# Kernel tuning notes

Hardware: AMD Instinct MI355X
Metric: run time of the kernel (lower is better)

## Reference

```python
import jax, jax.numpy as jnp
import numpy as np

B, T, DM, DFE, DH, DRH = 32, 2048, 128, 64, 64, 64
E, NF, NSF, TOPK = 8, 16, 64, 2
LN_EPS = 1e-5


def setup_inputs() -> dict:
    key = jax.random.key(0)
    ks = jax.random.split(key, 18)
    s = 0.05
    # base expert i owns columns [16*i, 16*i+16); scale=2 -> expert e uses base e//2
    expert_idx = jnp.asarray(np.stack([np.arange(NF) + NF * (e // 2) for e in range(E)]), dtype=jnp.int32)  # [E,NF]
    stage_idx = jnp.arange(NSF, dtype=jnp.int32)  # stage uses all 64 columns
    return {
        'hidden': jax.random.normal(ks[0], (B, T, DM), jnp.float32),
        'feat': jax.random.normal(ks[1], (B, T, NSF), jnp.float32),
        'ln_g': jnp.ones((DM,), jnp.float32),
        'ln_b': jnp.zeros((DM,), jnp.float32),
        'Wp': jax.random.normal(ks[2], (NSF, DFE), jnp.float32) * s,
        'bp': jnp.zeros((DFE,), jnp.float32),
        'Wr1': jax.random.normal(ks[3], (DM + DFE, DRH), jnp.float32) * s,
        'br1': jnp.zeros((DRH,), jnp.float32),
        'Wr2': jax.random.normal(ks[4], (DRH, E), jnp.float32) * s,
        'br2': jnp.zeros((E,), jnp.float32),
        'Wf': jax.random.normal(ks[5], (E, NF, DFE), jnp.float32) * s,
        'bf': jnp.zeros((E, DFE), jnp.float32),
        'We1h': jax.random.normal(ks[6], (E, DM, DH), jnp.float32) * s,
        'We1f': jax.random.normal(ks[7], (E, DFE, DH), jnp.float32) * s,
        'be1': jnp.zeros((E, DH), jnp.float32),
        'We2': jax.random.normal(ks[8], (E, DH, DM), jnp.float32) * s,
        'be2': jnp.zeros((E, DM), jnp.float32),
        'alpha': jnp.asarray(1.0, jnp.float32),
        'item_seq_len': jax.random.randint(ks[9], (B,), 1, T + 1),
        'expert_idx': expert_idx,
        'stage_idx': stage_idx,
    }


def _layernorm(x, g, b):
    mu = jnp.mean(x, -1, keepdims=True)
    v = jnp.mean(jnp.square(x - mu), -1, keepdims=True)
    return (x - mu) * jax.lax.rsqrt(v + LN_EPS) * g + b


def reference(hidden, feat, ln_g, ln_b, Wp, bp, Wr1, br1, Wr2, br2,
              Wf, bf, We1h, We1f, be1, We2, be2, alpha,
              item_seq_len, expert_idx, stage_idx):
    h = _layernorm(hidden, ln_g, ln_b)                         # [B,T,DM]  pre_ln
    femb = feat[..., stage_idx] @ Wp + bp                      # [B,T,DFE] stage feature projection
    # --- token router: MLP -> softmax(temp=1) -> top-k renormalized gates ---
    rin = jnp.concatenate([h, femb], -1)                       # [B,T,DM+DFE]
    logits = jax.nn.relu(rin @ Wr1 + br1) @ Wr2 + br2          # [B,T,E]
    probs = jax.nn.softmax(logits, axis=-1)
    topv, topi = jax.lax.top_k(probs, TOPK)                    # [B,T,K]
    topv = topv / jnp.sum(topv, -1, keepdims=True)
    gates = jnp.sum(jax.nn.one_hot(topi, E, dtype=probs.dtype) * topv[..., None], axis=-2)  # [B,T,E]
    valid = jnp.arange(T)[None, :] < item_seq_len[:, None]     # [B,T]
    gates = gates * valid[..., None].astype(gates.dtype)
    # --- experts: per-expert feature gather + 2-layer GELU MLP (hidden + feat inputs) ---
    ef = feat[:, :, expert_idx]                                # [B,T,E,NF] gather
    x = jnp.einsum('btef,efd->bted', ef, Wf) + bf              # [B,T,E,DFE]
    h1 = jax.nn.gelu(jnp.einsum('btd,edo->bteo', h, We1h)
                     + jnp.einsum('bted,edo->bteo', x, We1f) + be1, approximate=False)
    eo = jnp.einsum('bteo,eod->bted', h1, We2) + be2           # [B,T,E,DM]
    moe = jnp.einsum('bte,bted->btd', gates, eo)               # weighted combine
    next_hidden = hidden + alpha * moe                         # residual, alpha_scale=1, dropout=0
    return next_hidden, gates, probs
```

## Files before the change

kernel.cpp:

```cpp
#include <hip/hip_runtime.h>
#include <hip/hip_bf16.h>


typedef unsigned short u16;
typedef __attribute__((ext_vector_type(8))) short bfrag;
typedef __attribute__((ext_vector_type(8))) u16 u16x8;
typedef __attribute__((ext_vector_type(4))) float facc;
typedef __attribute__((ext_vector_type(4))) float f32x4;

#define NTOK 65536
#define CAP 65536

#define OFF_CNT   ((size_t)0)
#define OFF_FLG   ((size_t)64)
#define OFF_LTOK  ((size_t)512)
#define OFF_SMAPG (OFF_LTOK + (size_t)8*CAP*4)
#define OFF_HWS   (OFF_SMAPG + (size_t)NTOK*8)
#define OFF_EOTOK (OFF_HWS + (size_t)NTOK*128*2)
#define OFF_W1T   (OFF_EOTOK + (size_t)NTOK*2*128*2)
#define OFF_W2T   (OFF_W1T + 163840)
#define OFF_B1P   (OFF_W2T + 131072)
#define OFF_WPR   (OFF_B1P + 2048)
#define OFF_BR1P  (OFF_WPR + 16384)

__device__ __forceinline__ u16 f2bf(float f) {
  union { __hip_bfloat16 h; u16 u; } cv;
  cv.h = __float2bfloat16(f);
  return cv.u;
}
__device__ __forceinline__ float bf2f(u16 u) {
  return __uint_as_float(((unsigned)u) << 16);
}

__global__ __launch_bounds__(256)
void k0a_pre(const float* __restrict__ Wp, const float* __restrict__ bp,
             const float* __restrict__ Wr1, const float* __restrict__ br1,
             const float* __restrict__ Wf, const float* __restrict__ bfv,
             const float* __restrict__ We1h, const float* __restrict__ We1f,
             const float* __restrict__ be1, const float* __restrict__ We2,
             const int* __restrict__ eidx_g, const int* __restrict__ sidx_g,
             float* __restrict__ Wpr, float* __restrict__ br1p,
             u16* __restrict__ w1t, u16* __restrict__ w2t, float* __restrict__ b1p,
             int* __restrict__ flags)
{
  __shared__ float smA[64*68];
  __shared__ float smB[128*68];
  int b = blockIdx.x, tid = threadIdx.x;

  if (b == 0) {
    for (int idx = tid; idx < 4096; idx += 256) {
      int r = idx >> 6, c = idx & 63;
      smA[r*68 + c] = Wp[idx];
      smB[r*68 + c] = Wr1[128*64 + idx];
    }
    if (tid == 0) { int ok = 1; for (int i = 0; i < 64; ++i) ok &= (sidx_g[i] == i); flags[0] = ok; }
    __syncthreads();
    int i = tid >> 2, oq = (tid & 3) * 16;
    f32x4 acc[4];
    #pragma unroll
    for (int m = 0; m < 4; ++m) { f32x4 z = {0,0,0,0}; acc[m] = z; }
    for (int k = 0; k < 64; ++k) {
      float a = smA[i*68 + k];
      #pragma unroll
      for (int m = 0; m < 4; ++m) {
        f32x4 b4 = *(const f32x4*)(smB + k*68 + oq + m*4);
        #pragma unroll
        for (int j = 0; j < 4; ++j) acc[m][j] = fmaf(a, b4[j], acc[m][j]);
      }
    }
    #pragma unroll
    for (int m = 0; m < 4; ++m) *(f32x4*)(Wpr + i*64 + oq + m*4) = acc[m];
    if (tid < 64) {
      float s = br1[tid];
      for (int k = 0; k < 64; ++k) s = fmaf(bp[k], smB[k*68 + tid], s);
      br1p[tid] = s;
    }
  } else if (b <= 8) {
    int e = b - 1;
    for (int idx = tid; idx < 4096; idx += 256) {
      int r = idx >> 6, c = idx & 63;
      smB[r*68 + c] = We1f[e*4096 + idx];
    }
    for (int idx = tid; idx < 1024; idx += 256) {
      int r = idx >> 6, c = idx & 63;
      smA[r*68 + c] = Wf[e*1024 + idx];
    }
    if (tid == 0) {
      int s0 = eidx_g[e*16]; int ok = 1;
      for (int i = 0; i < 16; ++i) ok &= (eidx_g[e*16 + i] == s0 + i);
      flags[1 + e] = ok ? s0 : -1;
    }
    __syncthreads();
    int i = tid >> 4, jq = (tid & 15) * 4;
    f32x4 acc = {0,0,0,0};
    for (int d = 0; d < 64; ++d) {
      float a = smA[i*68 + d];
      f32x4 b4 = *(const f32x4*)(smB + d*68 + jq);
      #pragma unroll
      for (int j = 0; j < 4; ++j) acc[j] = fmaf(a, b4[j], acc[j]);
    }
    #pragma unroll
    for (int j = 0; j < 4; ++j) w1t[(size_t)(e*64 + jq + j)*160 + 128 + i] = f2bf(acc[j]);
    if (tid < 64) {
      float s = be1[e*64 + tid];
      for (int d = 0; d < 64; ++d) s = fmaf(bfv[e*64 + d], smB[d*68 + tid], s);
      b1p[e*64 + tid] = s;
    }
    for (int idx = tid; idx < 1024; idx += 256) {
      int jj = idx >> 4, kk = idx & 15;
      w1t[(size_t)(e*64 + jj)*160 + 144 + kk] = 0;
    }
  } else if (b <= 16) {
    int e = b - 9;
    for (int idx = tid; idx < 8192; idx += 256) {
      int r = idx >> 6, c = idx & 63;
      smB[r*68 + c] = We1h[(size_t)e*8192 + idx];
    }
    __syncthreads();
    int jj = tid & 63, kb = (tid >> 6) * 32;
    #pragma unroll
    for (int m = 0; m < 4; ++m) {
      u16x8 o;
      #pragma unroll
      for (int q = 0; q < 8; ++q) o[q] = f2bf(smB[(kb + m*8 + q)*68 + jj]);
      *(u16x8*)(w1t + (size_t)(e*64 + jj)*160 + kb + m*8) = o;
    }
  } else if (b <= 24) {
    int e = b - 17;
    for (int idx = tid; idx < 8192; idx += 256) {
      int r = idx >> 7, c = idx & 127;
      smB[r*132 + c] = We2[(size_t)e*8192 + idx];
    }
    __syncthreads();
    int d = tid & 127, kb = (tid >> 7) * 32;
    #pragma unroll
    for (int m = 0; m < 4; ++m) {
      u16x8 o;
      #pragma unroll
      for (int q = 0; q < 8; ++q) o[q] = f2bf(smB[(kb + m*8 + q)*132 + d]);
      *(u16x8*)(w2t + (size_t)(e*128 + d)*64 + kb + m*8) = o;
    }
  }
}

__global__ __launch_bounds__(256, 3)
void k1_router(const float* __restrict__ hidden, const float* __restrict__ feat,
               const float* __restrict__ ln_g, const float* __restrict__ ln_b,
               const float* __restrict__ Wr1, const float* __restrict__ Wr2,
               const float* __restrict__ br2, const int* __restrict__ seqlen,
               const int* __restrict__ sidx_g,
               const float* __restrict__ Wpr, const float* __restrict__ br1p,
               const int* __restrict__ flags,
               float* __restrict__ outG, float* __restrict__ outP,
               u16* __restrict__ hws, int* __restrict__ cnt,
               int* __restrict__ listTok, float* __restrict__ smapG)
{
  __shared__ __align__(16) char smemAt[64*128*4];
  __shared__ float Wc[64*64];
  __shared__ float sg[128], sb[128], sb1[64], sbr2[8];
  __shared__ int ssidx[64];
  __shared__ int lcnt[8], lbase[8];
  float* At = (float*)smemAt;
  int* ltok = (int*)smemAt;
  float* tgp = (float*)(smemAt + 4096);

  int tid = threadIdx.x;

  f32x4 wpf[4];
  #pragma unroll
  for (int u = 0; u < 4; ++u) wpf[u] = ((const f32x4*)Wpr)[u*256 + tid];

  if (tid < 128) sg[tid] = ln_g[tid]; else sb[tid-128] = ln_b[tid-128];
  if (tid < 64) { sb1[tid] = br1p[tid]; ssidx[tid] = sidx_g[tid]; }
  if (tid >= 64 && tid < 72) sbr2[tid-64] = br2[tid-64];
  if (tid >= 72 && tid < 80) lcnt[tid-72] = 0;
  int sidok = flags[0];

  int tl = tid >> 1, hq = tid & 1;
  int t = blockIdx.x * 128 + tl;

  f32x4 x[16];
  #pragma unroll
  for (int i = 0; i < 16; ++i) x[i] = *(const f32x4*)(hidden + (size_t)t*128 + hq*64 + i*4);
  float s = 0.f;
  #pragma unroll
  for (int i = 0; i < 16; ++i) { s += x[i][0] + x[i][1]; s += x[i][2] + x[i][3]; }
  s += __shfl_xor(s, 1, 64);
  float mu = s * (1.f/128.f);
  float v = 0.f;
  #pragma unroll
  for (int i = 0; i < 16; ++i) {
    #pragma unroll
    for (int j = 0; j < 4; ++j) { float d = x[i][j] - mu; v = fmaf(d, d, v); }
  }
  v += __shfl_xor(v, 1, 64);
  float rs = rsqrtf(v * (1.f/128.f) + 1e-5f);
  #pragma unroll
  for (int i = 0; i < 16; ++i) {
    #pragma unroll
    for (int j = 0; j < 4; ++j) {
      int c = hq*64 + i*4 + j;
      x[i][j] = (x[i][j] - mu) * rs * sg[c] + sb[c];
    }
  }
  #pragma unroll
  for (int m = 0; m < 8; ++m) {
    u16x8 o;
    #pragma unroll
    for (int j = 0; j < 4; ++j) { o[j] = f2bf(x[2*m][j]); o[4+j] = f2bf(x[2*m+1][j]); }
    *(u16x8*)(hws + (size_t)t*128 + hq*64 + m*8) = o;
  }
  int tb8 = tl >> 3, t7 = (tl & 7) << 2;
  if (sidok) {
    #pragma unroll
    for (int m = 0; m < 8; ++m) {
      f32x4 fv = *(const f32x4*)(feat + (size_t)t*64 + hq*32 + m*4);
      #pragma unroll
      for (int j = 0; j < 4; ++j) {
        int kr = hq*32 + m*4 + j;
        *(float*)((char*)At + (kr << 9) + (((tb8 ^ (kr & 15)) & 15) << 5) + t7) = fv[j];
      }
    }
  } else {
    #pragma unroll
    for (int i = 0; i < 32; ++i) {
      int kr = hq*32 + i;
      float fv = feat[(size_t)t*64 + ssidx[kr]];
      *(float*)((char*)At + (kr << 9) + (((tb8 ^ (kr & 15)) & 15) << 5) + t7) = fv;
    }
  }

  float acc[8][4];
  #pragma unroll
  for (int i = 0; i < 8; ++i)
    #pragma unroll
    for (int p = 0; p < 4; ++p) acc[i][p] = 0.f;

  int g8 = tid >> 4;
  int ob = (tid & 15) * 4;

  #pragma unroll 1
  for (int ci = 0; ci < 3; ++ci) {
    if (ci == 1 && hq == 0) {
      #pragma unroll
      for (int i = 0; i < 16; ++i)
        #pragma unroll
        for (int j = 0; j < 4; ++j) {
          int kr = i*4 + j;
          *(float*)((char*)At + (kr << 9) + (((tb8 ^ (kr & 15)) & 15) << 5) + t7) = x[i][j];
        }
    }
    if (ci == 2 && hq == 1) {
      #pragma unroll
      for (int i = 0; i < 16; ++i)
        #pragma unroll
        for (int j = 0; j < 4; ++j) {
          int kr = i*4 + j;
          *(float*)((char*)At + (kr << 9) + (((tb8 ^ (kr & 15)) & 15) << 5) + t7) = x[i][j];
        }
    }
    #pragma unroll
    for (int u = 0; u < 4; ++u) ((f32x4*)Wc)[u*256 + tid] = wpf[u];
    __syncthreads();
    if (ci < 2) {
      const f32x4* nsrc = (ci == 0) ? (const f32x4*)Wr1 : (const f32x4*)(Wr1 + 4096);
      #pragma unroll
      for (int u = 0; u < 4; ++u) wpf[u] = nsrc[u*256 + tid];
    }
    #pragma unroll 4
    for (int k = 0; k < 64; ++k) {
      int base = (k << 7) + (((g8 ^ (k & 15)) & 15) << 3);
      f32x4 a0 = *(const f32x4*)(At + base);
      f32x4 a1 = *(const f32x4*)(At + base + 4);
      f32x4 b4 = *(const f32x4*)(Wc + k*64 + ob);
      #pragma unroll
      for (int i = 0; i < 4; ++i)
        #pragma unroll
        for (int p = 0; p < 4; ++p) {
          acc[i][p]   = fmaf(a0[i], b4[p], acc[i][p]);
          acc[4+i][p] = fmaf(a1[i], b4[p], acc[4+i][p]);
        }
    }
    __syncthreads();
  }

  float w2r[4][8];
  #pragma unroll
  for (int p = 0; p < 4; ++p) {
    f32x4 wlo = *(const f32x4*)(Wr2 + (ob + p)*8);
    f32x4 whi = *(const f32x4*)(Wr2 + (ob + p)*8 + 4);
    #pragma unroll
    for (int e = 0; e < 4; ++e) { w2r[p][e] = wlo[e]; w2r[p][4+e] = whi[e]; }
  }
  float b1r[4];
  #pragma unroll
  for (int p = 0; p < 4; ++p) b1r[p] = sb1[ob + p];

  int j16 = tid & 15;
  #pragma unroll 1
  for (int ti = 0; ti < 8; ++ti) {
    float lo[8];
    #pragma unroll
    for (int e = 0; e < 8; ++e) lo[e] = 0.f;
    #pragma unroll
    for (int p = 0; p < 4; ++p) {
      float z = fmaxf(acc[ti][p] + b1r[p], 0.f);
      #pragma unroll
      for (int e = 0; e < 8; ++e) lo[e] = fmaf(z, w2r[p][e], lo[e]);
    }
    #pragma unroll
    for (int m = 1; m < 16; m <<= 1) {
      #pragma unroll
      for (int e = 0; e < 8; ++e) lo[e] += __shfl_xor(lo[e], m, 64);
    }
    #pragma unroll
    for (int e = 0; e < 8; ++e) lo[e] += sbr2[e];

    int tloc = g8*8 + ti;
    int tt = blockIdx.x*128 + tloc;
    float mx = lo[0];
    #pragma unroll
    for (int e = 1; e < 8; ++e) mx = fmaxf(mx, lo[e]);
    float ex[8]; float ss = 0.f;
    #pragma unroll
    for (int e = 0; e < 8; ++e) { ex[e] = __expf(lo[e] - mx); ss += ex[e]; }
    float inv = 1.f / ss;
    float p[8];
    #pragma unroll
    for (int e = 0; e < 8; ++e) p[e] = ex[e] * inv;
    float p1 = p[0]; int i1 = 0;
    #pragma unroll
    for (int e = 1; e < 8; ++e) { bool tk2 = p[e] > p1; p1 = tk2 ? p[e] : p1; i1 = tk2 ? e : i1; }
    float p2 = -1.f; int i2 = 0;
    #pragma unroll
    for (int e = 0; e < 8; ++e) { bool tk2 = (e != i1) && (p[e] > p2); p2 = tk2 ? p[e] : p2; i2 = tk2 ? e : i2; }
    bool valid = (tt & 2047) < seqlen[tt >> 11];
    float gden = 1.f / (p1 + p2);
    float g1 = p1 * gden, g2 = p2 * gden;
    float pv = p[0];
    #pragma unroll
    for (int e = 1; e < 8; ++e) pv = (j16 == e) ? p[e] : pv;
    if (j16 < 8) outP[(size_t)tt*8 + j16] = pv;
    float gv = (j16 == i1) ? g1 : ((j16 == i2) ? g2 : 0.f);
    if (!valid) gv = 0.f;
    if (j16 < 8) outG[(size_t)tt*8 + j16] = gv;
    if (j16 == 0) {
      if (valid) {
        int lp = atomicAdd(&lcnt[i1], 1); if (lp < 128) ltok[i1*128 + lp] = (tt << 1);
        lp = atomicAdd(&lcnt[i2], 1);     if (lp < 128) ltok[i2*128 + lp] = (tt << 1) | 1;
        tgp[tloc*2] = g1; tgp[tloc*2+1] = g2;
      } else {
        tgp[tloc*2] = 0.f; tgp[tloc*2+1] = 0.f;
      }
    }
  }

  __syncthreads();
  if (tid < 8) { int n8 = min(lcnt[tid], 128); lbase[tid] = atomicAdd(&cnt[tid], n8); }
  __syncthreads();
  #pragma unroll 1
  for (int e = 0; e < 8; ++e) {
    int ncnt = min(lcnt[e], 128);
    if (tid < ncnt) listTok[(size_t)e*CAP + lbase[e] + tid] = ltok[e*128 + tid];
  }
  if (tid < 128) {
    float2 g; g.x = tgp[tid*2]; g.y = tgp[tid*2+1];
    ((float2*)smapG)[blockIdx.x*128 + tid] = g;
  }
}

__global__ __launch_bounds__(256)
void k2_experts(const float* __restrict__ feat, const u16* __restrict__ hws,
                const u16* __restrict__ w1t, const u16* __restrict__ w2t,
                const float* __restrict__ b1p, const float* __restrict__ be2,
                const int* __restrict__ eidx_g, const int* __restrict__ cnt,
                const int* __restrict__ listTok, const int* __restrict__ flags,
                u16* __restrict__ eoTok)
{
  __shared__ u16 Xs[64*168];
  __shared__ u16 H1s[64*88];
  __shared__ float b1s[64], be2s[128];
  __shared__ int sent[64];
  __shared__ int seidx[16];
  __shared__ int snr;

  int b = blockIdx.x, tid = threadIdx.x;
  int e = -1, row0 = 0, n = 0, accb = 0;
  #pragma unroll
  for (int i = 0; i < 8; ++i) {
    int ci = cnt[i]; int ns = (ci + 63) >> 6;
    if (e < 0 && b < accb + ns) { e = i; row0 = (b - accb) << 6; n = ci; }
    accb += ns;
  }
  if (e < 0) return;
  int nr = n - row0; if (nr > 64) nr = 64;
  if (tid == 0) snr = nr;
  int fb = flags[1 + e];

  if (tid < 64) {
    int ent = (tid < nr) ? listTok[(size_t)e*CAP + row0 + tid] : 0;
    sent[tid] = ent;
    b1s[tid] = b1p[e*64 + tid];
  } else if (tid < 192) {
    be2s[tid - 64] = be2[e*128 + tid - 64];
  } else if (tid < 208) {
    seidx[tid-192] = eidx_g[e*16 + tid - 192];
  }
  __syncthreads();

  for (int c2 = tid; c2 < 1024; c2 += 256) {
    int r = c2 >> 4, p = c2 & 15;
    u16x8 vv = *(const u16x8*)(hws + (size_t)(sent[r] >> 1)*128 + p*8);
    *(u16x8*)((char*)Xs + r*336 + p*16) = vv;
  }
  if (tid < 128) {
    int r = tid >> 1, hf = tid & 1;
    int tk = sent[r] >> 1;
    u16x8 ov;
    if (fb >= 0) {
      f32x4 v0 = *(const f32x4*)(feat + (size_t)tk*64 + fb + hf*8);
      f32x4 v1 = *(const f32x4*)(feat + (size_t)tk*64 + fb + hf*8 + 4);
      #pragma unroll
      for (int q = 0; q < 4; ++q) { ov[q] = f2bf(v0[q]); ov[4+q] = f2bf(v1[q]); }
    } else {
      #pragma unroll
      for (int q = 0; q < 8; ++q) ov[q] = f2bf(feat[(size_t)tk*64 + seidx[hf*8 + q]]);
    }
    *(u16x8*)((char*)Xs + r*336 + 256 + hf*16) = ov;
    u16x8 zv = {0,0,0,0,0,0,0,0};
    *(u16x8*)((char*)Xs + r*336 + 288 + hf*16) = zv;
  }
  __syncthreads();

  int w = tid >> 6, lane = tid & 63;
  int la = lane & 15, lg = lane >> 4;
  const u16* w1e = w1t + (size_t)e*64*160;
  const u16* w2e = w2t + (size_t)e*128*64;

  facc acc[4];
  #pragma unroll
  for (int ni = 0; ni < 4; ++ni) { facc z = {0.f,0.f,0.f,0.f}; acc[ni] = z; }
  #pragma unroll
  for (int kc = 0; kc < 5; ++kc) {
    int r = w*16 + la;
    bfrag af = *(const bfrag*)((const char*)Xs + r*336 + kc*64 + lg*16);
    #pragma unroll
    for (int ni = 0; ni < 4; ++ni) {
      bfrag bf2 = *(const bfrag*)(w1e + (size_t)(ni*16 + la)*160 + kc*32 + lg*8);
      acc[ni] = __builtin_amdgcn_mfma_f32_16x16x32_bf16(af, bf2, acc[ni], 0, 0, 0);
    }
  }
  #pragma unroll
  for (int ni = 0; ni < 4; ++ni)
    #pragma unroll
    for (int rg = 0; rg < 4; ++rg) {
      int r = w*16 + lg*4 + rg;
      int c = ni*16 + la;
      float z = acc[ni][rg] + b1s[c];
      float gl = 0.5f * z * (1.f + erff(z * 0.70710678118f));
      *(u16*)((char*)H1s + r*176 + c*2) = f2bf(gl);
    }
  __syncthreads();

  facc acc2[8];
  #pragma unroll
  for (int ni = 0; ni < 8; ++ni) { facc z = {0.f,0.f,0.f,0.f}; acc2[ni] = z; }
  #pragma unroll
  for (int kc = 0; kc < 2; ++kc) {
    int r = w*16 + la;
    bfrag af = *(const bfrag*)((const char*)H1s + r*176 + kc*64 + lg*16);
    #pragma unroll
    for (int ni = 0; ni < 8; ++ni) {
      bfrag bf2 = *(const bfrag*)(w2e + (size_t)(ni*16 + la)*64 + kc*32 + lg*8);
      acc2[ni] = __builtin_amdgcn_mfma_f32_16x16x32_bf16(af, bf2, acc2[ni], 0, 0, 0);
    }
  }
  #pragma unroll
  for (int ni = 0; ni < 8; ++ni)
    #pragma unroll
    for (int rg = 0; rg < 4; ++rg) {
      int r = w*16 + lg*4 + rg;
      int c = ni*16 + la;
      if (r < snr) {
        float vv = acc2[ni][rg] + be2s[c];
        eoTok[(size_t)sent[r]*128 + c] = f2bf(vv);
      }
    }
}

__global__ __launch_bounds__(256)
void k3_combine(const float* __restrict__ hidden, const float* __restrict__ smapG,
                const u16* __restrict__ eoTok, const float* __restrict__ alphap,
                float* __restrict__ outN)
{
  int tid = threadIdx.x;
  int tok = tid >> 2, q = tid & 3;
  int t = blockIdx.x*64 + tok;
  float2 g = ((const float2*)smapG)[t];
  float a = alphap[0];
  float ag0 = a * g.x, ag1 = a * g.y;
  const f32x4* hp = (const f32x4*)(hidden + (size_t)t*128 + q*32);
  f32x4* op = (f32x4*)(outN + (size_t)t*128 + q*32);
  const u16x8* e0 = (const u16x8*)(eoTok + ((size_t)t*2)*128 + q*32);
  const u16x8* e1 = (const u16x8*)(eoTok + ((size_t)t*2 + 1)*128 + q*32);
  #pragma unroll
  for (int i = 0; i < 4; ++i) {
    f32x4 r0 = hp[2*i], r1 = hp[2*i+1];
    if (g.x != 0.f) {
      u16x8 x0 = e0[i];
      #pragma unroll
      for (int j = 0; j < 4; ++j) { r0[j] = fmaf(ag0, bf2f(x0[j]), r0[j]); r1[j] = fmaf(ag0, bf2f(x0[4+j]), r1[j]); }
    }
    if (g.y != 0.f) {
      u16x8 x1 = e1[i];
      #pragma unroll
      for (int j = 0; j < 4; ++j) { r0[j] = fmaf(ag1, bf2f(x1[j]), r0[j]); r1[j] = fmaf(ag1, bf2f(x1[4+j]), r1[j]); }
    }
    op[2*i] = r0; op[2*i+1] = r1;
  }
}

extern "C" void kernel_launch(void* const* d_in, const int* in_sizes, int n_in,
                              void* d_out, int out_size, void* d_ws, size_t ws_size,
                              hipStream_t stream) {
  const float* hidden = (const float*)d_in[0];
  const float* feat   = (const float*)d_in[1];
  const float* ln_g   = (const float*)d_in[2];
  const float* ln_b   = (const float*)d_in[3];
  const float* Wp     = (const float*)d_in[4];
  const float* bp     = (const float*)d_in[5];
  const float* Wr1    = (const float*)d_in[6];
  const float* br1    = (const float*)d_in[7];
  const float* Wr2    = (const float*)d_in[8];
  const float* br2    = (const float*)d_in[9];
  const float* Wf     = (const float*)d_in[10];
  const float* bfv    = (const float*)d_in[11];
  const float* We1h   = (const float*)d_in[12];
  const float* We1f   = (const float*)d_in[13];
  const float* be1    = (const float*)d_in[14];
  const float* We2    = (const float*)d_in[15];
  const float* be2    = (const float*)d_in[16];
  const float* alpha  = (const float*)d_in[17];
  const int* seqlen   = (const int*)d_in[18];
  const int* eidx     = (const int*)d_in[19];
  const int* sidx     = (const int*)d_in[20];

  char* ws = (char*)d_ws;
  int*   cnt      = (int*)(ws + OFF_CNT);
  int*   flags    = (int*)(ws + OFF_FLG);
  int*   listTok  = (int*)(ws + OFF_LTOK);
  float* smapG    = (float*)(ws + OFF_SMAPG);
  u16*   hws      = (u16*)(ws + OFF_HWS);
  u16*   eoTok    = (u16*)(ws + OFF_EOTOK);
  u16*   w1t      = (u16*)(ws + OFF_W1T);
  u16*   w2t      = (u16*)(ws + OFF_W2T);
  float* b1p      = (float*)(ws + OFF_B1P);
  float* Wpr      = (float*)(ws + OFF_WPR);
  float* br1p     = (float*)(ws + OFF_BR1P);

  float* outN = (float*)d_out;
  float* outG = outN + (size_t)NTOK * 128;
  float* outP = outG + (size_t)NTOK * 8;

  hipMemsetAsync(ws + OFF_CNT, 0, 256, stream);
  k0a_pre<<<25, 256, 0, stream>>>(Wp, bp, Wr1, br1, Wf, bfv, We1h, We1f, be1, We2,
                                  eidx, sidx, Wpr, br1p, w1t, w2t, b1p, flags);
  k1_router<<<512, 256, 0, stream>>>(hidden, feat, ln_g, ln_b, Wr1, Wr2, br2, seqlen,
                                     sidx, Wpr, br1p, flags, outG, outP, hws, cnt,
                                     listTok, smapG);
  k2_experts<<<2056, 256, 0, stream>>>(feat, hws, w1t, w2t, b1p, be2, eidx,
                                       cnt, listTok, flags, eoTok);
  k3_combine<<<1024, 256, 0, stream>>>(hidden, smapG, eoTok, alpha, outN);
}
```

Baseline: 135.0 us.

## Restructure router kernel to 64 tokens per block with split-K across waves

The router kernel now handles 64 tokens per block instead of 128 and launches twice as many blocks. Each wave owns 16 of the 64 hidden units and reads its weights straight from global memory instead of staging them in shared memory. Partial logits from the four waves are reduced through shared memory, and a single wave then does softmax, top-k and vectorized output writes. The aim is higher occupancy and less shared-memory and shuffle traffic. The costs are repeated global or L2 weight loads in every block and an epilogue where only one wave is busy.

```diff
diff --git a/kernel.cpp b/kernel.cpp
--- a/kernel.cpp
+++ b/kernel.cpp
@@ -143,7 +143,7 @@
   }
 }
 
-__global__ __launch_bounds__(256, 3)
+__global__ __launch_bounds__(256, 4)
 void k1_router(const float* __restrict__ hidden, const float* __restrict__ feat,
                const float* __restrict__ ln_g, const float* __restrict__ ln_b,
                const float* __restrict__ Wr1, const float* __restrict__ Wr2,
@@ -155,217 +155,201 @@
                u16* __restrict__ hws, int* __restrict__ cnt,
                int* __restrict__ listTok, float* __restrict__ smapG)
 {
-  __shared__ __align__(16) char smemAt[64*128*4];
-  __shared__ float Wc[64*64];
-  __shared__ float sg[128], sb[128], sb1[64], sbr2[8];
+  __shared__ float At[64*64];
+  __shared__ float plo[64*33 + 4];
+  __shared__ float sg[128], sb[128];
   __shared__ int ssidx[64];
   __shared__ int lcnt[8], lbase[8];
-  float* At = (float*)smemAt;
-  int* ltok = (int*)smemAt;
-  float* tgp = (float*)(smemAt + 4096);
+  __shared__ int ltok[8][64];
 
   int tid = threadIdx.x;
-
-  f32x4 wpf[4];
-  #pragma unroll
-  for (int u = 0; u < 4; ++u) wpf[u] = ((const f32x4*)Wpr)[u*256 + tid];
-
   if (tid < 128) sg[tid] = ln_g[tid]; else sb[tid-128] = ln_b[tid-128];
-  if (tid < 64) { sb1[tid] = br1p[tid]; ssidx[tid] = sidx_g[tid]; }
-  if (tid >= 64 && tid < 72) sbr2[tid-64] = br2[tid-64];
-  if (tid >= 72 && tid < 80) lcnt[tid-72] = 0;
+  if (tid < 64) ssidx[tid] = sidx_g[tid];
+  if (tid >= 128 && tid < 136) lcnt[tid-128] = 0;
   int sidok = flags[0];
 
-  int tl = tid >> 1, hq = tid & 1;
-  int t = blockIdx.x * 128 + tl;
-
-  f32x4 x[16];
-  #pragma unroll
-  for (int i = 0; i < 16; ++i) x[i] = *(const f32x4*)(hidden + (size_t)t*128 + hq*64 + i*4);
+  int tok = tid >> 2, q = tid & 3;
+  int t = blockIdx.x * 64 + tok;
+
+  f32x4 x[8];
+  #pragma unroll
+  for (int i = 0; i < 8; ++i) x[i] = *(const f32x4*)(hidden + (size_t)t*128 + q*32 + i*4);
   float s = 0.f;
   #pragma unroll
-  for (int i = 0; i < 16; ++i) { s += x[i][0] + x[i][1]; s += x[i][2] + x[i][3]; }
-  s += __shfl_xor(s, 1, 64);
+  for (int i = 0; i < 8; ++i) { s += x[i][0] + x[i][1]; s += x[i][2] + x[i][3]; }
+  s += __shfl_xor(s, 1, 64); s += __shfl_xor(s, 2, 64);
   float mu = s * (1.f/128.f);
   float v = 0.f;
   #pragma unroll
-  for (int i = 0; i < 16; ++i) {
+  for (int i = 0; i < 8; ++i) {
     #pragma unroll
     for (int j = 0; j < 4; ++j) { float d = x[i][j] - mu; v = fmaf(d, d, v); }
   }
-  v += __shfl_xor(v, 1, 64);
+  v += __shfl_xor(v, 1, 64); v += __shfl_xor(v, 2, 64);
   float rs = rsqrtf(v * (1.f/128.f) + 1e-5f);
   #pragma unroll
-  for (int i = 0; i < 16; ++i) {
+  for (int i = 0; i < 8; ++i) {
     #pragma unroll
     for (int j = 0; j < 4; ++j) {
-      int c = hq*64 + i*4 + j;
+      int c = q*32 + i*4 + j;
       x[i][j] = (x[i][j] - mu) * rs * sg[c] + sb[c];
     }
   }
   #pragma unroll
-  for (int m = 0; m < 8; ++m) {
+  for (int m = 0; m < 4; ++m) {
     u16x8 o;
     #pragma unroll
     for (int j = 0; j < 4; ++j) { o[j] = f2bf(x[2*m][j]); o[4+j] = f2bf(x[2*m+1][j]); }
-    *(u16x8*)(hws + (size_t)t*128 + hq*64 + m*8) = o;
-  }
-  int tb8 = tl >> 3, t7 = (tl & 7) << 2;
+    *(u16x8*)(hws + (size_t)t*128 + q*32 + m*8) = o;
+  }
+  float fv[16];
   if (sidok) {
     #pragma unroll
-    for (int m = 0; m < 8; ++m) {
-      f32x4 fv = *(const f32x4*)(feat + (size_t)t*64 + hq*32 + m*4);
+    for (int m = 0; m < 4; ++m) {
+      f32x4 f4 = *(const f32x4*)(feat + (size_t)t*64 + q*16 + m*4);
+      #pragma unroll
+      for (int j = 0; j < 4; ++j) fv[m*4+j] = f4[j];
+    }
+  } else {
+    #pragma unroll
+    for (int i = 0; i < 16; ++i) fv[i] = feat[(size_t)t*64 + ssidx[q*16 + i]];
+  }
+
+  int lane = tid & 63;
+  int w = tid >> 6;
+  int wo = __builtin_amdgcn_readfirstlane(w * 16);
+
+  float acc[16];
+  #pragma unroll
+  for (int j = 0; j < 16; ++j) acc[j] = 0.f;
+
+  #pragma unroll 1
+  for (int c = 0; c < 3; ++c) {
+    if (c == 0) {
+      if (q < 2) {
+        #pragma unroll
+        for (int i = 0; i < 8; ++i)
+          #pragma unroll
+          for (int j = 0; j < 4; ++j) {
+            int r = q*32 + i*4 + j;
+            At[(r << 6) + (tok ^ r)] = x[i][j];
+          }
+      }
+    } else if (c == 1) {
+      if (q >= 2) {
+        #pragma unroll
+        for (int i = 0; i < 8; ++i)
+          #pragma unroll
+          for (int j = 0; j < 4; ++j) {
+            int r = (q-2)*32 + i*4 + j;
+            At[(r << 6) + (tok ^ r)] = x[i][j];
+          }
+      }
+    } else {
+      #pragma unroll
+      for (int i = 0; i < 16; ++i) {
+        int r = q*16 + i;
+        At[(r << 6) + (tok ^ r)] = fv[i];
+      }
+    }
+    __syncthreads();
+    const float* wsrc = (c == 0) ? Wr1 : (c == 1) ? (Wr1 + 4096) : Wpr;
+    #pragma unroll 16
+    for (int k = 0; k < 64; ++k) {
+      float xk = At[(k << 6) + (lane ^ k)];
+      const f32x4* wr = (const f32x4*)(wsrc + (k << 6) + wo);
+      f32x4 w0 = wr[0], w1 = wr[1], w2 = wr[2], w3 = wr[3];
       #pragma unroll
       for (int j = 0; j < 4; ++j) {
-        int kr = hq*32 + m*4 + j;
-        *(float*)((char*)At + (kr << 9) + (((tb8 ^ (kr & 15)) & 15) << 5) + t7) = fv[j];
-      }
-    }
-  } else {
-    #pragma unroll
-    for (int i = 0; i < 32; ++i) {
-      int kr = hq*32 + i;
-      float fv = feat[(size_t)t*64 + ssidx[kr]];
-      *(float*)((char*)At + (kr << 9) + (((tb8 ^ (kr & 15)) & 15) << 5) + t7) = fv;
-    }
-  }
-
-  float acc[8][4];
-  #pragma unroll
-  for (int i = 0; i < 8; ++i)
-    #pragma unroll
-    for (int p = 0; p < 4; ++p) acc[i][p] = 0.f;
-
-  int g8 = tid >> 4;
-  int ob = (tid & 15) * 4;
-
-  #pragma unroll 1
-  for (int ci = 0; ci < 3; ++ci) {
-    if (ci == 1 && hq == 0) {
-      #pragma unroll
-      for (int i = 0; i < 16; ++i)
-        #pragma unroll
-        for (int j = 0; j < 4; ++j) {
-          int kr = i*4 + j;
-          *(float*)((char*)At + (kr << 9) + (((tb8 ^ (kr & 15)) & 15) << 5) + t7) = x[i][j];
-        }
-    }
-    if (ci == 2 && hq == 1) {
-      #pragma unroll
-      for (int i = 0; i < 16; ++i)
-        #pragma unroll
-        for (int j = 0; j < 4; ++j) {
-          int kr = i*4 + j;
-          *(float*)((char*)At + (kr << 9) + (((tb8 ^ (kr & 15)) & 15) << 5) + t7) = x[i][j];
-        }
-    }
-    #pragma unroll
-    for (int u = 0; u < 4; ++u) ((f32x4*)Wc)[u*256 + tid] = wpf[u];
+        acc[j]    = fmaf(w0[j], xk, acc[j]);
+        acc[4+j]  = fmaf(w1[j], xk, acc[4+j]);
+        acc[8+j]  = fmaf(w2[j], xk, acc[8+j]);
+        acc[12+j] = fmaf(w3[j], xk, acc[12+j]);
+      }
+    }
     __syncthreads();
-    if (ci < 2) {
-      const f32x4* nsrc = (ci == 0) ? (const f32x4*)Wr1 : (const f32x4*)(Wr1 + 4096);
-      #pragma unroll
-      for (int u = 0; u < 4; ++u) wpf[u] = nsrc[u*256 + tid];
-    }
-    #pragma unroll 4
-    for (int k = 0; k < 64; ++k) {
-      int base = (k << 7) + (((g8 ^ (k & 15)) & 15) << 3);
-      f32x4 a0 = *(const f32x4*)(At + base);
-      f32x4 a1 = *(const f32x4*)(At + base + 4);
-      f32x4 b4 = *(const f32x4*)(Wc + k*64 + ob);
-      #pragma unroll
-      for (int i = 0; i < 4; ++i)
-        #pragma unroll
-        for (int p = 0; p < 4; ++p) {
-          acc[i][p]   = fmaf(a0[i], b4[p], acc[i][p]);
-          acc[4+i][p] = fmaf(a1[i], b4[p], acc[4+i][p]);
-        }
-    }
-    __syncthreads();
-  }
-
-  float w2r[4][8];
-  #pragma unroll
-  for (int p = 0; p < 4; ++p) {
-    f32x4 wlo = *(const f32x4*)(Wr2 + (ob + p)*8);
-    f32x4 whi = *(const f32x4*)(Wr2 + (ob + p)*8 + 4);
-    #pragma unroll
-    for (int e = 0; e < 4; ++e) { w2r[p][e] = wlo[e]; w2r[p][4+e] = whi[e]; }
-  }
-  float b1r[4];
-  #pragma unroll
-  for (int p = 0; p < 4; ++p) b1r[p] = sb1[ob + p];
-
-  int j16 = tid & 15;
-  #pragma unroll 1
-  for (int ti = 0; ti < 8; ++ti) {
+  }
+
+  {
     float lo[8];
     #pragma unroll
     for (int e = 0; e < 8; ++e) lo[e] = 0.f;
-    #pragma unroll
-    for (int p = 0; p < 4; ++p) {
-      float z = fmaxf(acc[ti][p] + b1r[p], 0.f);
-      #pragma unroll
-      for (int e = 0; e < 8; ++e) lo[e] = fmaf(z, w2r[p][e], lo[e]);
-    }
-    #pragma unroll
-    for (int m = 1; m < 16; m <<= 1) {
-      #pragma unroll
-      for (int e = 0; e < 8; ++e) lo[e] += __shfl_xor(lo[e], m, 64);
-    }
-    #pragma unroll
-    for (int e = 0; e < 8; ++e) lo[e] += sbr2[e];
-
-    int tloc = g8*8 + ti;
-    int tt = blockIdx.x*128 + tloc;
-    float mx = lo[0];
-    #pragma unroll
-    for (int e = 1; e < 8; ++e) mx = fmaxf(mx, lo[e]);
+    const f32x4* b1v = (const f32x4*)(br1p + wo);
+    f32x4 b0 = b1v[0], b1 = b1v[1], b2 = b1v[2], b3 = b1v[3];
+    #pragma unroll
+    for (int j = 0; j < 16; ++j) {
+      float bj = (j < 4) ? b0[j & 3] : (j < 8) ? b1[j & 3] : (j < 12) ? b2[j & 3] : b3[j & 3];
+      float zj = fmaxf(acc[j] + bj, 0.f);
+      const f32x4* w2p = (const f32x4*)(Wr2 + (wo + j)*8);
+      f32x4 wa = w2p[0], wb = w2p[1];
+      #pragma unroll
+      for (int e = 0; e < 4; ++e) {
+        lo[e]   = fmaf(zj, wa[e], lo[e]);
+        lo[4+e] = fmaf(zj, wb[e], lo[4+e]);
+      }
+    }
+    #pragma unroll
+    for (int e = 0; e < 8; ++e) plo[lane*33 + w*8 + e] = lo[e];
+  }
+  __syncthreads();
+
+  if (w == 0) {
+    int tt = blockIdx.x*64 + lane;
+    float L[8];
+    #pragma unroll
+    for (int e = 0; e < 8; ++e)
+      L[e] = plo[lane*33 + e] + plo[lane*33 + 8 + e] + plo[lane*33 + 16 + e]
+           + plo[lane*33 + 24 + e] + br2[e];
+    float mx = L[0];
+    #pragma unroll
+    for (int e = 1; e < 8; ++e) mx = fmaxf(mx, L[e]);
     float ex[8]; float ss = 0.f;
     #pragma unroll
-    for (int e = 0; e < 8; ++e) { ex[e] = __expf(lo[e] - mx); ss += ex[e]; }
+    for (int e = 0; e < 8; ++e) { ex[e] = __expf(L[e] - mx); ss += ex[e]; }
     float inv = 1.f / ss;
     float p[8];
     #pragma unroll
     for (int e = 0; e < 8; ++e) p[e] = ex[e] * inv;
     float p1 = p[0]; int i1 = 0;
     #pragma unroll
-    for (int e = 1; e < 8; ++e) { bool tk2 = p[e] > p1; p1 = tk2 ? p[e] : p1; i1 = tk2 ? e : i1; }
+    for (int e = 1; e < 8; ++e) { bool tk = p[e] > p1; p1 = tk ? p[e] : p1; i1 = tk ? e : i1; }
     float p2 = -1.f; int i2 = 0;
     #pragma unroll
-    for (int e = 0; e < 8; ++e) { bool tk2 = (e != i1) && (p[e] > p2); p2 = tk2 ? p[e] : p2; i2 = tk2 ? e : i2; }
+    for (int e = 0; e < 8; ++e) { bool tk = (e != i1) && (p[e] > p2); p2 = tk ? p[e] : p2; i2 = tk ? e : i2; }
     bool valid = (tt & 2047) < seqlen[tt >> 11];
     float gden = 1.f / (p1 + p2);
     float g1 = p1 * gden, g2 = p2 * gden;
-    float pv = p[0];
-    #pragma unroll
-    for (int e = 1; e < 8; ++e) pv = (j16 == e) ? p[e] : pv;
-    if (j16 < 8) outP[(size_t)tt*8 + j16] = pv;
-    float gv = (j16 == i1) ? g1 : ((j16 == i2) ? g2 : 0.f);
-    if (!valid) gv = 0.f;
-    if (j16 < 8) outG[(size_t)tt*8 + j16] = gv;
-    if (j16 == 0) {
-      if (valid) {
-        int lp = atomicAdd(&lcnt[i1], 1); if (lp < 128) ltok[i1*128 + lp] = (tt << 1);
-        lp = atomicAdd(&lcnt[i2], 1);     if (lp < 128) ltok[i2*128 + lp] = (tt << 1) | 1;
-        tgp[tloc*2] = g1; tgp[tloc*2+1] = g2;
-      } else {
-        tgp[tloc*2] = 0.f; tgp[tloc*2+1] = 0.f;
-      }
-    }
-  }
-
+
+    f32x4 pa, pb;
+    #pragma unroll
+    for (int e = 0; e < 4; ++e) { pa[e] = p[e]; pb[e] = p[4+e]; }
+    *(f32x4*)(outP + (size_t)tt*8)     = pa;
+    *(f32x4*)(outP + (size_t)tt*8 + 4) = pb;
+
+    f32x4 ga, gb;
+    #pragma unroll
+    for (int e = 0; e < 4; ++e) {
+      ga[e] = valid ? ((e == i1) ? g1 : (e == i2) ? g2 : 0.f) : 0.f;
+      gb[e] = valid ? ((e+4 == i1) ? g1 : (e+4 == i2) ? g2 : 0.f) : 0.f;
+    }
+    *(f32x4*)(outG + (size_t)tt*8)     = ga;
+    *(f32x4*)(outG + (size_t)tt*8 + 4) = gb;
+
+    float2 gm; gm.x = valid ? g1 : 0.f; gm.y = valid ? g2 : 0.f;
+    ((float2*)smapG)[tt] = gm;
+
+    if (valid) {
+      int lp = atomicAdd(&lcnt[i1], 1); ltok[i1][lp] = (tt << 1);
+      lp = atomicAdd(&lcnt[i2], 1);     ltok[i2][lp] = (tt << 1) | 1;
+    }
+  }
   __syncthreads();
-  if (tid < 8) { int n8 = min(lcnt[tid], 128); lbase[tid] = atomicAdd(&cnt[tid], n8); }
+  if (tid < 8) lbase[tid] = atomicAdd(&cnt[tid], lcnt[tid]);
   __syncthreads();
   #pragma unroll 1
   for (int e = 0; e < 8; ++e) {
-    int ncnt = min(lcnt[e], 128);
-    if (tid < ncnt) listTok[(size_t)e*CAP + lbase[e] + tid] = ltok[e*128 + tid];
-  }
-  if (tid < 128) {
-    float2 g; g.x = tgp[tid*2]; g.y = tgp[tid*2+1];
-    ((float2*)smapG)[blockIdx.x*128 + tid] = g;
+    int ncnt = lcnt[e];
+    if (tid < ncnt) listTok[(size_t)e*CAP + lbase[e] + tid] = ltok[e][tid];
   }
 }
 
@@ -421,10 +405,10 @@
       f32x4 v0 = *(const f32x4*)(feat + (size_t)tk*64 + fb + hf*8);
       f32x4 v1 = *(const f32x4*)(feat + (size_t)tk*64 + fb + hf*8 + 4);
       #pragma unroll
-      for (int q = 0; q < 4; ++q) { ov[q] = f2bf(v0[q]); ov[4+q] = f2bf(v1[q]); }
+      for (int p = 0; p < 4; ++p) { ov[p] = f2bf(v0[p]); ov[4+p] = f2bf(v1[p]); }
     } else {
       #pragma unroll
-      for (int q = 0; q < 8; ++q) ov[q] = f2bf(feat[(size_t)tk*64 + seidx[hf*8 + q]]);
+      for (int p = 0; p < 8; ++p) ov[p] = f2bf(feat[(size_t)tk*64 + seidx[hf*8 + p]]);
     }
     *(u16x8*)((char*)Xs + r*336 + 256 + hf*16) = ov;
     u16x8 zv = {0,0,0,0,0,0,0,0};
@@ -565,9 +549,9 @@
   hipMemsetAsync(ws + OFF_CNT, 0, 256, stream);
   k0a_pre<<<25, 256, 0, stream>>>(Wp, bp, Wr1, br1, Wf, bfv, We1h, We1f, be1, We2,
                                   eidx, sidx, Wpr, br1p, w1t, w2t, b1p, flags);
-  k1_router<<<512, 256, 0, stream>>>(hidden, feat, ln_g, ln_b, Wr1, Wr2, br2, seqlen,
-                                     sidx, Wpr, br1p, flags, outG, outP, hws, cnt,
-                                     listTok, smapG);
+  k1_router<<<1024, 256, 0, stream>>>(hidden, feat, ln_g, ln_b, Wr1, Wr2, br2, seqlen,
+                                      sidx, Wpr, br1p, flags, outG, outP, hws, cnt,
+                                      listTok, smapG);
   k2_experts<<<2056, 256, 0, stream>>>(feat, hws, w1t, w2t, b1p, be2, eidx,
                                        cnt, listTok, flags, eoTok);
   k3_combine<<<1024, 256, 0, stream>>>(hidden, smapG, eoTok, alpha, outN);
```

Measured after the change: 152.6 us. +13.0%, slower.
